# Optimization experiments

Hardware: AMD Instinct MI355X
Metric: run time of the kernel (lower is better)

The kernel has to match this reference:

```python
import jax, jax.numpy as jnp
import numpy as np

B, S, D_MODEL, N_HEADS, D_FF = 4, 2048, 1024, 16, 4096
HEAD_DIM = D_MODEL // N_HEADS
NUM_BUCKETS, MAX_DISTANCE = 32, 128
EPS = 1e-6


def _relative_position_bucket(relative_position, num_buckets=NUM_BUCKETS, max_distance=MAX_DISTANCE):
    # bidirectional (encoder) variant, matching T5RelativePositionBias
    n = -relative_position
    nb = num_buckets // 2
    ret = (n < 0).astype(jnp.int32) * nb
    n = jnp.abs(n)
    max_exact = nb // 2
    val_if_large = max_exact + (
        jnp.log(jnp.maximum(n, 1).astype(jnp.float32) / max_exact)
        / np.log(max_distance / max_exact) * (nb - max_exact)
    ).astype(jnp.int32)
    val_if_large = jnp.minimum(val_if_large, nb - 1)
    return ret + jnp.where(n < max_exact, n, val_if_large)


def t5_position_bias(rel_emb, q_len, k_len):
    ctx = jnp.arange(q_len)[:, None]
    mem = jnp.arange(k_len)[None, :]
    rp_bucket = _relative_position_bucket(mem - ctx)          # [S, S]
    bias = rel_emb[rp_bucket]                                  # [S, S, H]
    return jnp.transpose(bias, (2, 0, 1))[None]                # [1, H, S, S]


def layer_norm(x, g, b):
    mu = jnp.mean(x, axis=-1, keepdims=True)
    var = jnp.mean(jnp.square(x - mu), axis=-1, keepdims=True)
    return (x - mu) * jax.lax.rsqrt(var + EPS) * g + b


def setup_inputs() -> dict:
    key = jax.random.key(0)
    ks = jax.random.split(key, 20)
    s = 0.02
    p = {
        'src': jax.random.normal(ks[0], (B, S, D_MODEL), jnp.float32),
        'wq': jax.random.normal(ks[1], (D_MODEL, D_MODEL), jnp.float32) * s,
        'bq': jnp.zeros((D_MODEL,), jnp.float32),
        'wk': jax.random.normal(ks[2], (D_MODEL, D_MODEL), jnp.float32) * s,
        'bk': jnp.zeros((D_MODEL,), jnp.float32),
        'wv': jax.random.normal(ks[3], (D_MODEL, D_MODEL), jnp.float32) * s,
        'bv': jnp.zeros((D_MODEL,), jnp.float32),
        'wo': jax.random.normal(ks[4], (D_MODEL, D_MODEL), jnp.float32) * s,
        'bo': jnp.zeros((D_MODEL,), jnp.float32),
        'w1': jax.random.normal(ks[5], (D_MODEL, D_FF), jnp.float32) * s,
        'b1': jnp.zeros((D_FF,), jnp.float32),
        'w2': jax.random.normal(ks[6], (D_FF, D_MODEL), jnp.float32) * s,
        'b2': jnp.zeros((D_MODEL,), jnp.float32),
        'ln1_g': jnp.ones((D_MODEL,), jnp.float32),
        'ln1_b': jnp.zeros((D_MODEL,), jnp.float32),
        'ln2_g': jnp.ones((D_MODEL,), jnp.float32),
        'ln2_b': jnp.zeros((D_MODEL,), jnp.float32),
        'rel_emb': jax.random.normal(ks[7], (NUM_BUCKETS, N_HEADS), jnp.float32) * s,
    }
    return p


def reference(src, wq, bq, wk, bk, wv, bv, wo, bo, w1, b1, w2, b2,
              ln1_g, ln1_b, ln2_g, ln2_b, rel_emb):
    b, s, _ = src.shape

    # --- self-attention block (pre-norm) ---
    xn = layer_norm(src, ln1_g, ln1_b)
    q = (xn @ wq + bq).reshape(b, s, N_HEADS, HEAD_DIM).transpose(0, 2, 1, 3)
    k = (xn @ wk + bk).reshape(b, s, N_HEADS, HEAD_DIM).transpose(0, 2, 1, 3)
    v = (xn @ wv + bv).reshape(b, s, N_HEADS, HEAD_DIM).transpose(0, 2, 1, 3)

    bias = t5_position_bias(rel_emb, s, s)                       # [1,H,S,S]
    scores = jnp.einsum('bhqd,bhkd->bhqk', q, k) / np.sqrt(HEAD_DIM) + bias
    attn = jax.nn.softmax(scores, axis=-1)
    ctx = jnp.einsum('bhqk,bhkd->bhqd', attn, v)                 # [B,H,S,Dh]
    ctx = ctx.transpose(0, 2, 1, 3).reshape(b, s, D_MODEL)
    x = src + (ctx @ wo + bo)

    # --- FFN block (pre-norm, ReLU) ---
    yn = layer_norm(x, ln2_g, ln2_b)
    y = jax.nn.relu(yn @ w1 + b1) @ w2 + b2
    return x + y
```

## Files before the change

### kernel.cpp

```cpp
#include <hip/hip_runtime.h>
#include <math.h>

typedef unsigned short u16;

#define S_LEN 2048
#define BSZ 4
#define DM 1024
#define NH 16
#define HD 64
#define DFF 4096
#define ROWS (BSZ * S_LEN)
#define LOG2E 1.4426950408889634f

typedef __attribute__((__ext_vector_type__(8))) __bf16 bf16x8;
typedef __attribute__((__ext_vector_type__(8))) short short8;
typedef __attribute__((__ext_vector_type__(4))) short short4v;
typedef __attribute__((__ext_vector_type__(4))) float f32x4;
typedef __attribute__((__ext_vector_type__(4))) float float4v;

__device__ __forceinline__ float bf2f(u16 u) {
    union { unsigned int i; float f; } c; c.i = ((unsigned int)u) << 16; return c.f;
}
__device__ __forceinline__ u16 f2bf(float f) {
    union { float f; unsigned int i; } c; c.f = f;
    unsigned int r = c.i + 0x7fffu + ((c.i >> 16) & 1u);
    return (u16)(r >> 16);
}
__device__ __forceinline__ u16 f2bf_cvt(float f) {
    __bf16 h = (__bf16)f;
    return __builtin_bit_cast(u16, h);
}
__device__ __forceinline__ float ldin(const void* p, long i, int f32) {
    return f32 ? ((const float*)p)[i] : bf2f(((const u16*)p)[i]);
}
__device__ __forceinline__ int dtype_f32(const u16* ln1g) {
    return ln1g[0] != 0x3F80;
}
__device__ __forceinline__ void gl_lds16(const void* g, void* l) {
    __builtin_amdgcn_global_load_lds(
        (const __attribute__((address_space(1))) unsigned int*)g,
        (__attribute__((address_space(3))) unsigned int*)l, 16, 0, 0);
}

#define BARR  asm volatile("s_barrier" ::: "memory")
#define LGKM0 asm volatile("s_waitcnt lgkmcnt(0)" ::: "memory")
#define VM4   asm volatile("s_waitcnt vmcnt(4)" ::: "memory")
#define VM2   asm volatile("s_waitcnt vmcnt(2)" ::: "memory")
#define VM0   asm volatile("s_waitcnt vmcnt(0)" ::: "memory")

__device__ __forceinline__ void tr_tile(
    const void* __restrict__ src, u16* __restrict__ dst, int N, int K,
    int bx, int by, int f32, int tid, u16 (*t)[72])
{
#pragma unroll
    for (int i = 0; i < 2; i++) {
        int c = tid + i * 256;
        int row = c >> 3, col = (c & 7) * 8;
        long off = (long)(by * 64 + row) * N + bx * 64 + col;
        short8 v;
        if (f32) {
            const float* s = (const float*)src + off;
            float4v a = *(const float4v*)s;
            float4v b = *(const float4v*)(s + 4);
#pragma unroll
            for (int k = 0; k < 4; k++) { v[k] = (short)f2bf(a[k]); v[k + 4] = (short)f2bf(b[k]); }
        } else {
            v = *(const short8*)((const u16*)src + off);
        }
        *(short8*)(&t[row][col]) = v;
    }
    __syncthreads();
#pragma unroll
    for (int i = 0; i < 2; i++) {
        int c = tid + i * 256;
        int row = c >> 3, col = (c & 7) * 8;
        short8 v;
#pragma unroll
        for (int jj = 0; jj < 8; jj++) v[jj] = (short)t[col + jj][row];
        *(short8*)(dst + (long)(bx * 64 + row) * K + by * 64 + col) = v;
    }
}

__global__ __launch_bounds__(256) void prep_all(
    const void* wq, const void* wk, const void* wv, const void* wo,
    const void* w1, const void* w2,
    const void* bq, const void* bk, const void* bv, const void* bo,
    const void* b1, const void* b2, const void* l1g, const void* l1b,
    const void* l2g, const void* l2b, const void* rel,
    const void* src, u16* __restrict__ xn,
    u16* __restrict__ wqkvt, u16* __restrict__ wot,
    u16* __restrict__ w1t, u16* __restrict__ w2t,
    u16* __restrict__ smalls, float* __restrict__ bias_full)
{
    __shared__ u16 t[64][72];
    __shared__ float ps1[4], ps2[4];
    int z = blockIdx.z;
    int f32 = dtype_f32((const u16*)l1g);

    if (z < 4) {
        if (blockIdx.x >= 16) return;
        const void* s = (z == 0) ? wq : (z == 1) ? wk : (z == 2) ? wv : wo;
        u16* dst = (z < 3) ? wqkvt + (long)z * 1024 * 1024 : wot;
        tr_tile(s, dst, DM, DM, blockIdx.x, blockIdx.y, f32, threadIdx.x, t);
        return;
    }
    if (z == 4) {
        tr_tile(w1, w1t, DFF, DM, blockIdx.x, blockIdx.y, f32, threadIdx.x, t);
        return;
    }
    if (z == 5) {
        tr_tile(w2, w2t, DM, DFF, blockIdx.y, blockIdx.x, f32, threadIdx.x, t);
        return;
    }
    if (z == 6) {
        int bidx = blockIdx.y * 64 + blockIdx.x;
        if (bidx >= 256) return;
        int tid = bidx * 256 + threadIdx.x;
        if (tid < 13312) {
            float v;
            if      (tid < 1024)  v = ldin(bq,  tid,         f32);
            else if (tid < 2048)  v = ldin(bk,  tid - 1024,  f32);
            else if (tid < 3072)  v = ldin(bv,  tid - 2048,  f32);
            else if (tid < 4096)  v = ldin(bo,  tid - 3072,  f32);
            else if (tid < 8192)  v = ldin(b1,  tid - 4096,  f32);
            else if (tid < 9216)  v = ldin(b2,  tid - 8192,  f32);
            else if (tid < 10240) v = ldin(l1g, tid - 9216,  f32);
            else if (tid < 11264) v = ldin(l1b, tid - 10240, f32);
            else if (tid < 12288) v = ldin(l2g, tid - 11264, f32);
            else                  v = ldin(l2b, tid - 12288, f32);
            smalls[tid] = f2bf(v);
        }
        if (tid < 4095 * 16) {
            int dIdx = tid >> 4;
            int h = tid & 15;
            int delta = dIdx - 2047;
            int n = -delta;
            int ret = (n < 0) ? 16 : 0;
            int na = (n < 0) ? -n : n;
            int bkt;
            if (na < 8) {
                bkt = na;
            } else {
                float tval = logf((float)na * 0.125f) * 2.8853900817779268f;
                int v = 8 + (int)tval;
                bkt = v < 15 ? v : 15;
            }
            bkt += ret;
            bias_full[h * 4095 + dIdx] = ldin(rel, bkt * 16 + h, f32) * LOG2E;
        }
        return;
    }
    {
        int row = (z - 7) * 1024 + blockIdx.y * 64 + blockIdx.x;
        int tid = threadIdx.x;
        float vals[4];
        if (f32) {
            float4v v = *(const float4v*)((const float*)src + (long)row * DM + tid * 4);
#pragma unroll
            for (int k = 0; k < 4; k++) vals[k] = v[k];
        } else {
            short4v v = *(const short4v*)((const u16*)src + (long)row * DM + tid * 4);
#pragma unroll
            for (int k = 0; k < 4; k++) vals[k] = bf2f((u16)v[k]);
        }
        float s1 = 0.f, s2 = 0.f;
#pragma unroll
        for (int k = 0; k < 4; k++) { s1 += vals[k]; s2 += vals[k] * vals[k]; }
#pragma unroll
        for (int off = 32; off > 0; off >>= 1) {
            s1 += __shfl_xor(s1, off);
            s2 += __shfl_xor(s2, off);
        }
        int wave = tid >> 6, lane = tid & 63;
        if (lane == 0) { ps1[wave] = s1; ps2[wave] = s2; }
        __syncthreads();
        s1 = ps1[0] + ps1[1] + ps1[2] + ps1[3];
        s2 = ps2[0] + ps2[1] + ps2[2] + ps2[3];
        float mu = s1 * (1.0f / DM);
        float var = s2 * (1.0f / DM) - mu * mu;
        float rs = rsqrtf(var + 1e-6f);
        short4v ov;
#pragma unroll
        for (int k = 0; k < 4; k++) {
            float gv = ldin(l1g, tid * 4 + k, f32);
            float bv = ldin(l1b, tid * 4 + k, f32);
            ov[k] = (short)f2bf((vals[k] - mu) * rs * gv + bv);
        }
        *(short4v*)(xn + (long)row * DM + tid * 4) = ov;
    }
}

__global__ __launch_bounds__(256) void ln_kernel(
    const void* __restrict__ xin, int external, const u16* __restrict__ ln1g,
    const u16* __restrict__ g, const u16* __restrict__ bta, u16* __restrict__ out)
{
    int f32 = external ? dtype_f32(ln1g) : 0;
    int row = blockIdx.x;
    int tid = threadIdx.x;
    float vals[4];
    if (f32) {
        float4v v = *(const float4v*)((const float*)xin + (long)row * DM + tid * 4);
#pragma unroll
        for (int k = 0; k < 4; k++) vals[k] = v[k];
    } else {
        short4v v = *(const short4v*)((const u16*)xin + (long)row * DM + tid * 4);
#pragma unroll
        for (int k = 0; k < 4; k++) vals[k] = bf2f((u16)v[k]);
    }
    float s1 = 0.f, s2 = 0.f;
#pragma unroll
    for (int k = 0; k < 4; k++) { s1 += vals[k]; s2 += vals[k] * vals[k]; }
#pragma unroll
    for (int off = 32; off > 0; off >>= 1) {
        s1 += __shfl_xor(s1, off);
        s2 += __shfl_xor(s2, off);
    }
    __shared__ float ps1[4], ps2[4];
    int wave = tid >> 6, lane = tid & 63;
    if (lane == 0) { ps1[wave] = s1; ps2[wave] = s2; }
    __syncthreads();
    s1 = ps1[0] + ps1[1] + ps1[2] + ps1[3];
    s2 = ps2[0] + ps2[1] + ps2[2] + ps2[3];
    float mu = s1 * (1.0f / DM);
    float var = s2 * (1.0f / DM) - mu * mu;
    float rs = rsqrtf(var + 1e-6f);
    short4v ov;
#pragma unroll
    for (int k = 0; k < 4; k++) {
        float gv = bf2f(g[tid * 4 + k]);
        float bv = bf2f(bta[tid * 4 + k]);
        ov[k] = (short)f2bf((vals[k] - mu) * rs * gv + bv);
    }
    *(short4v*)(out + (long)row * DM + tid * 4) = ov;
}

#define TM 256
#define TN 256
#define TK 64

#define PHASE(bi, q, STAGE, WAITV)                                             \
    {                                                                          \
        if ((q) == 0) {                                                        \
            _Pragma("unroll")                                                  \
            for (int j = 0; j < 4; j++) {                                      \
                _Pragma("unroll")                                              \
                for (int t = 0; t < 2; t++)                                    \
                    bfr[j][t] = __builtin_bit_cast(bf16x8, *(const short8*)(   \
                        &Bs[bi][wn * 64 + j * 16 + l16][((t * 4 + quad) ^ rxor) * 8])); \
            }                                                                  \
        }                                                                      \
        _Pragma("unroll")                                                      \
        for (int i = 0; i < 2; i++) {                                          \
            _Pragma("unroll")                                                  \
            for (int t = 0; t < 2; t++)                                        \
                af[i][t] = __builtin_bit_cast(bf16x8, *(const short8*)(        \
                    &As[bi][wm * 128 + ((q) * 2 + i) * 16 + l16][((t * 4 + quad) ^ rxor) * 8])); \
        }                                                                      \
        STAGE                                                                  \
        WAITV;                                                                 \
        BARR;                                                                  \
        LGKM0;                                                                 \
        __builtin_amdgcn_sched_barrier(0);                                     \
        __builtin_amdgcn_s_setprio(1);                                         \
        _Pragma("unroll")                                                      \
        for (int i = 0; i < 2; i++) {                                          \
            _Pragma("unroll")                                                  \
            for (int j = 0; j < 4; j++) {                                      \
                acc[(q) * 2 + i][j] = __builtin_amdgcn_mfma_f32_16x16x32_bf16( \
                    af[i][0], bfr[j][0], acc[(q) * 2 + i][j], 0, 0, 0);        \
                acc[(q) * 2 + i][j] = __builtin_amdgcn_mfma_f32_16x16x32_bf16( \
                    af[i][1], bfr[j][1], acc[(q) * 2 + i][j], 0, 0, 0);        \
            }                                                                  \
        }                                                                      \
        __builtin_amdgcn_s_setprio(0);                                         \
        BARR;                                                                  \
    }

__global__ __launch_bounds__(512, 2) void gemm256(
    const u16* __restrict__ A, const u16* __restrict__ Bt,
    const u16* __restrict__ bias, int M, int N, int K, int mode,
    u16* __restrict__ out_q, u16* __restrict__ out_k, u16* __restrict__ out_v,
    u16* __restrict__ outp)
{
    __shared__ u16 As[2][TM][TK];
    __shared__ u16 Bs[2][TN][TK];

    int tid = threadIdx.x;
    int wavei = tid >> 6, lane = tid & 63;
    int quad = lane >> 4, l16 = lane & 15;
    int wm = wavei >> 2, wn = wavei & 3;

    int nwg = gridDim.x * gridDim.y;
    int bid = blockIdx.y * gridDim.x + blockIdx.x;
    int chunk = nwg >> 3;
    int swz = (bid & 7) * chunk + (bid >> 3);
    int bx = swz % gridDim.x, by = swz / gridDim.x;
    long m0 = (long)by * TM, n0 = (long)bx * TN;

    int srow = tid >> 3;
    int pchk = tid & 7;
    int cchk = pchk ^ (srow & 7);
    int rxor = l16 & 7;

    int NT = K / TK;

    auto stageA = [&](int bufi, int h, int t) {
        const u16* g = A + (m0 + h * 128 + srow) * (long)K + (long)t * TK + cchk * 8;
        gl_lds16(g,                 &As[bufi][h * 128 + srow     ][pchk * 8]);
        gl_lds16(g + 64 * (long)K,  &As[bufi][h * 128 + srow + 64][pchk * 8]);
    };
    auto stageB = [&](int bufi, int h, int t) {
        const u16* g = Bt + (n0 + h * 128 + srow) * (long)K + (long)t * TK + cchk * 8;
        gl_lds16(g,                 &Bs[bufi][h * 128 + srow     ][pchk * 8]);
        gl_lds16(g + 64 * (long)K,  &Bs[bufi][h * 128 + srow + 64][pchk * 8]);
    };

    f32x4 acc[8][4];
    f32x4 z = {0.f, 0.f, 0.f, 0.f};
#pragma unroll
    for (int i = 0; i < 8; i++)
#pragma unroll
        for (int j = 0; j < 4; j++) acc[i][j] = z;

    bf16x8 bfr[4][2];
    bf16x8 af[2][2];

    stageA(0, 0, 0); stageA(0, 1, 0); stageB(0, 0, 0); stageB(0, 1, 0);
    stageB(1, 0, 1); stageB(1, 1, 1);
    VM4;
    BARR;

    for (int kt = 0; kt < NT - 2; kt += 2) {
        PHASE(0, 0, { stageA(1, 0, kt + 1); stageA(1, 1, kt + 1); }, (void)0);
        PHASE(0, 1, { stageB(0, 0, kt + 2); }, (void)0);
        PHASE(0, 2, { stageB(0, 1, kt + 2); }, (void)0);
        PHASE(0, 3, {}, VM4);
        PHASE(1, 0, { stageA(0, 0, kt + 2); }, (void)0);
        PHASE(1, 1, { stageA(0, 1, kt + 2); stageB(1, 0, kt + 3); }, (void)0);
        PHASE(1, 2, { stageB(1, 1, kt + 3); }, (void)0);
        PHASE(1, 3, {}, VM4);
    }
    PHASE(0, 0, { stageA(1, 0, NT - 1); stageA(1, 1, NT - 1); }, (void)0);
    PHASE(0, 1, {}, (void)0);
    PHASE(0, 2, {}, (void)0);
    PHASE(0, 3, {}, VM0);
    PHASE(1, 0, {}, (void)0);
    PHASE(1, 1, {}, (void)0);
    PHASE(1, 2, {}, (void)0);
    PHASE(1, 3, {}, (void)0);

#pragma unroll
    for (int i = 0; i < 8; i++) {
#pragma unroll
        for (int j = 0; j < 4; j++) {
            long gr0 = m0 + wm * 128 + i * 16 + quad * 4;
            long gc = n0 + wn * 64 + j * 16 + l16;
            float bsv = bf2f(bias[gc]);
            if (mode == 1) {
                int sel = (int)(gc >> 10);
                int cc = (int)(gc & 1023);
                int h = cc >> 6, d = cc & 63;
                int b = (int)(gr0 >> 11), s0 = (int)(gr0 & 2047);
                if (sel == 2) {
                    short4v pk;
#pragma unroll
                    for (int r = 0; r < 4; r++)
                        pk[r] = (short)f2bf_cvt(acc[i][j][r] + bsv);
                    *(short4v*)(out_v +
                        (((long)(b * NH + h)) * HD + d) * S_LEN + s0) = pk;
                } else {
                    u16* dst = (sel == 0) ? out_q : out_k;
#pragma unroll
                    for (int r = 0; r < 4; r++)
                        dst[(((long)(b * NH + h)) * S_LEN + s0 + r) * HD + d] =
                            f2bf_cvt(acc[i][j][r] + bsv);
                }
            } else {
#pragma unroll
                for (int r = 0; r < 4; r++) {
                    float val = acc[i][j][r] + bsv;
                    outp[(gr0 + r) * (long)N + gc] = f2bf_cvt(val > 0.f ? val : 0.f);
                }
            }
        }
    }
}

#define NBM 256
#define NBN 128

#define PHN(bi, half, STAGE, WAITV)                                            \
    {                                                                          \
        if ((half) == 0) {                                                     \
            _Pragma("unroll")                                                  \
            for (int j = 0; j < 2; j++) {                                      \
                _Pragma("unroll")                                              \
                for (int t = 0; t < 2; t++)                                    \
                    nbfr[j][t] = __builtin_bit_cast(bf16x8, *(const short8*)(  \
                        &Bs[bi][wn * 32 + j * 16 + l16][((t * 4 + quad) ^ rxor) * 8])); \
            }                                                                  \
        }                                                                      \
        _Pragma("unroll")                                                      \
        for (int i = 0; i < 4; i++) {                                          \
            _Pragma("unroll")                                                  \
            for (int t = 0; t < 2; t++)                                        \
                naf[i][t] = __builtin_bit_cast(bf16x8, *(const short8*)(       \
                    &As[bi][wm * 128 + ((half) * 4 + i) * 16 + l16][((t * 4 + quad) ^ rxor) * 8])); \
        }                                                                      \
        STAGE                                                                  \
        WAITV;                                                                 \
        BARR;                                                                  \
        LGKM0;                                                                 \
        __builtin_amdgcn_sched_barrier(0);                                     \
        __builtin_amdgcn_s_setprio(1);                                         \
        _Pragma("unroll")                                                      \
        for (int i = 0; i < 4; i++) {                                          \
            _Pragma("unroll")                                                  \
            for (int j = 0; j < 2; j++) {                                      \
                acc[(half) * 4 + i][j] = __builtin_amdgcn_mfma_f32_16x16x32_bf16( \
                    naf[i][0], nbfr[j][0], acc[(half) * 4 + i][j], 0, 0, 0);   \
                acc[(half) * 4 + i][j] = __builtin_amdgcn_mfma_f32_16x16x32_bf16( \
                    naf[i][1], nbfr[j][1], acc[(half) * 4 + i][j], 0, 0, 0);   \
            }                                                                  \
        }                                                                      \
        __builtin_amdgcn_s_setprio(0);                                         \
        BARR;                                                                  \
    }

__global__ __launch_bounds__(512, 2) void gemm256n(
    const u16* __restrict__ A, const u16* __restrict__ Bt,
    const u16* __restrict__ bias, int M, int N, int K, int mode,
    const void* __restrict__ res, void* __restrict__ outp,
    const u16* __restrict__ ln1g)
{
    __shared__ u16 As[2][NBM][TK];
    __shared__ u16 Bs[2][NBN][TK];

    int tid = threadIdx.x;
    int wavei = tid >> 6, lane = tid & 63;
    int quad = lane >> 4, l16 = lane & 15;
    int wm = wavei >> 2, wn = wavei & 3;

    int nwg = gridDim.x * gridDim.y;
    int bid = blockIdx.y * gridDim.x + blockIdx.x;
    int chunk = nwg >> 3;
    int swz = (bid & 7) * chunk + (bid >> 3);
    int bx = swz % gridDim.x, by = swz / gridDim.x;
    long m0 = (long)by * NBM, n0 = (long)bx * NBN;
    int flg = dtype_f32(ln1g);

    int srow = tid >> 3;
    int pchk = tid & 7;
    int cchk = pchk ^ (srow & 7);
    int rxor = l16 & 7;

    int NT = K / TK;

    auto stageA = [&](int bufi, int h, int t) {
        const u16* g = A + (m0 + h * 128 + srow) * (long)K + (long)t * TK + cchk * 8;
        gl_lds16(g,                 &As[bufi][h * 128 + srow     ][pchk * 8]);
        gl_lds16(g + 64 * (long)K,  &As[bufi][h * 128 + srow + 64][pchk * 8]);
    };
    auto stageB = [&](int bufi, int t) {
        const u16* g = Bt + (n0 + srow) * (long)K + (long)t * TK + cchk * 8;
        gl_lds16(g,                 &Bs[bufi][srow     ][pchk * 8]);
        gl_lds16(g + 64 * (long)K,  &Bs[bufi][srow + 64][pchk * 8]);
    };

    f32x4 acc[8][2];
    f32x4 z = {0.f, 0.f, 0.f, 0.f};
#pragma unroll
    for (int i = 0; i < 8; i++)
#pragma unroll
        for (int j = 0; j < 2; j++) acc[i][j] = z;

    bf16x8 nbfr[2][2];
    bf16x8 naf[4][2];

    stageA(0, 0, 0); stageA(0, 1, 0); stageB(0, 0);
    stageB(1, 1);
    VM2;
    BARR;

    for (int kt = 0; kt < NT - 2; kt += 2) {
        PHN(0, 0, { stageA(1, 0, kt + 1); stageA(1, 1, kt + 1); }, (void)0);
        PHN(0, 1, { stageB(0, kt + 2); }, VM2);
        PHN(1, 0, { stageA(0, 0, kt + 2); stageA(0, 1, kt + 2); }, (void)0);
        PHN(1, 1, { stageB(1, kt + 3); }, VM2);
    }
    PHN(0, 0, { stageA(1, 0, NT - 1); stageA(1, 1, NT - 1); }, (void)0);
    PHN(0, 1, {}, VM0);
    PHN(1, 0, {}, (void)0);
    PHN(1, 1, {}, (void)0);

#pragma unroll
    for (int i = 0; i < 8; i++) {
#pragma unroll
        for (int j = 0; j < 2; j++) {
#pragma unroll
            for (int r = 0; r < 4; r++) {
                long gr = m0 + wm * 128 + i * 16 + quad * 4 + r;
                long gc = n0 + wn * 32 + j * 16 + l16;
                float val = acc[i][j][r] + bf2f(bias[gc]);
                long idx = gr * (long)N + gc;
                if (mode == 2) {
                    float rv = flg ? ((const float*)res)[idx]
                                   : bf2f(((const u16*)res)[idx]);
                    ((u16*)outp)[idx] = f2bf_cvt(val + rv);
                } else {
                    float o = val + bf2f(((const u16*)res)[idx]);
                    if (flg) ((float*)outp)[idx] = o;
                    else     ((u16*)outp)[idx]  = f2bf_cvt(o);
                }
            }
        }
    }
}

__global__ __launch_bounds__(512, 4) void attn_kernel(
    const u16* __restrict__ Qg, const u16* __restrict__ Kg, const u16* __restrict__ Vtg,
    const float* __restrict__ bias_full, u16* __restrict__ ctx)
{
    __shared__ u16 Ks[64][64];
    __shared__ u16 Vt[64][64];
    __shared__ u16 Ps[128][76];
    __shared__ u16 bias_s[2176];

    int nwg = gridDim.x * gridDim.y;
    int bid = blockIdx.y * gridDim.x + blockIdx.x;
    int chunk = nwg >> 3;
    int swz = (bid & 7) * chunk + (bid >> 3);
    int qt = swz % gridDim.x, bh = swz / gridDim.x;

    int b = bh >> 4, h = bh & 15;
    int q0 = qt * 128;
    const u16* Q  = Qg  + (long)bh * S_LEN * HD;
    const u16* Kp = Kg  + (long)bh * S_LEN * HD;
    const u16* Vp = Vtg + (long)bh * HD * S_LEN;

    int tid = threadIdx.x;
    int wave = tid >> 6, lane = tid & 63;
    int quad = lane >> 4, l16 = lane & 15;

    for (int i = tid; i < 2176; i += 512)
        bias_s[i] = f2bf(bias_full[h * 4095 + 1920 + i - q0]);
    float Bneg = bias_full[h * 4095 + 0];
    float Bpos = bias_full[h * 4095 + 4094];

    int isv = wave >= 4;
    int t2 = tid & 255;
    int prow = t2 >> 3, pchk = t2 & 7;
    int cchk = pchk ^ (prow & 7);
    int rxor = l16 & 7;
    int rc0 = (quad ^ rxor) * 8;
    int rc1 = ((4 + quad) ^ rxor) * 8;

    bf16x8 aq[2];
#pragma unroll
    for (int t = 0; t < 2; t++)
        aq[t] = __builtin_bit_cast(bf16x8,
            *(const short8*)(Q + (long)(q0 + wave * 16 + l16) * HD + t * 32 + quad * 8));

    bf16x8 ones;
#pragma unroll
    for (int i = 0; i < 8; i++) ones[i] = (__bf16)1.0f;

    f32x4 o[4];
    f32x4 z = {0.f, 0.f, 0.f, 0.f};
#pragma unroll
    for (int j = 0; j < 4; j++) o[j] = z;
    f32x4 lacc = z;

    int ib = 127 + quad * 4 - wave * 16 - l16;
    const float c0 = 0.125f * LOG2E;

    auto compute = [&](int t0) {
        f32x4 s_[4];
#pragma unroll
        for (int j = 0; j < 4; j++) {
            f32x4 a = z;
            bf16x8 kf0 = __builtin_bit_cast(bf16x8, *(const short8*)(&Ks[j * 16 + l16][rc0]));
            a = __builtin_amdgcn_mfma_f32_16x16x32_bf16(kf0, aq[0], a, 0, 0, 0);
            bf16x8 kf1 = __builtin_bit_cast(bf16x8, *(const short8*)(&Ks[j * 16 + l16][rc1]));
            a = __builtin_amdgcn_mfma_f32_16x16x32_bf16(kf1, aq[1], a, 0, 0, 0);
            s_[j] = a;
        }
        int d0 = t0 - q0;
        int nearb = (d0 >= -153 && d0 <= 217);
        float bconst = (d0 > 0) ? Bpos : Bneg;
#pragma unroll
        for (int j = 0; j < 4; j++) {
            short4v pk;
#pragma unroll
            for (int r = 0; r < 4; r++) {
                float bl = nearb ? bf2f(bias_s[ib + t0 + j * 16 + r]) : bconst;
                float p = __builtin_amdgcn_exp2f(fmaf(s_[j][r], c0, bl));
                pk[r] = (short)f2bf_cvt(p);
            }
            *(short4v*)(&Ps[wave * 16 + l16][j * 16 + quad * 4]) = pk;
        }
        bf16x8 ap[2];
#pragma unroll
        for (int tt = 0; tt < 2; tt++)
            ap[tt] = __builtin_bit_cast(bf16x8,
                *(const short8*)(&Ps[wave * 16 + l16][tt * 32 + quad * 8]));
        lacc = __builtin_amdgcn_mfma_f32_16x16x32_bf16(ap[0], ones, lacc, 0, 0, 0);
        lacc = __builtin_amdgcn_mfma_f32_16x16x32_bf16(ap[1], ones, lacc, 0, 0, 0);
#pragma unroll
        for (int j = 0; j < 4; j++) {
            f32x4 t = o[j];
            bf16x8 bv0 = __builtin_bit_cast(bf16x8, *(const short8*)(&Vt[j * 16 + l16][rc0]));
            t = __builtin_amdgcn_mfma_f32_16x16x32_bf16(ap[0], bv0, t, 0, 0, 0);
            bf16x8 bv1 = __builtin_bit_cast(bf16x8, *(const short8*)(&Vt[j * 16 + l16][rc1]));
            t = __builtin_amdgcn_mfma_f32_16x16x32_bf16(ap[1], bv1, t, 0, 0, 0);
            o[j] = t;
        }
    };

    auto ld0 = [&](int t) -> short8 {
        return isv ? *(const short8*)(Vp + (long)prow * S_LEN + t + cchk * 8)
                   : *(const short8*)(Kp + (long)(t + prow) * HD + cchk * 8);
    };
    auto ld1 = [&](int t) -> short8 {
        return isv ? *(const short8*)(Vp + (long)(32 + prow) * S_LEN + t + cchk * 8)
                   : *(const short8*)(Kp + (long)(t + 32 + prow) * HD + cchk * 8);
    };
    u16* dst0 = isv ? &Vt[prow][pchk * 8] : &Ks[prow][pchk * 8];
    u16* dst1 = isv ? &Vt[32 + prow][pchk * 8] : &Ks[32 + prow][pchk * 8];

    short8 sa0 = ld0(0), sa1 = ld1(0);
    short8 sb0, sb1;

    for (int t0 = 0; t0 < S_LEN; t0 += 128) {
        if (t0 > 0) BARR;
        VM0;
        *(short8*)dst0 = sa0;
        *(short8*)dst1 = sa1;
        sb0 = ld0(t0 + 64);
        sb1 = ld1(t0 + 64);
        LGKM0; BARR;
        compute(t0);

        BARR;
        VM0;
        *(short8*)dst0 = sb0;
        *(short8*)dst1 = sb1;
        if (t0 + 128 < S_LEN) {
            sa0 = ld0(t0 + 128);
            sa1 = ld1(t0 + 128);
        }
        LGKM0; BARR;
        compute(t0 + 64);
    }

#pragma unroll
    for (int r = 0; r < 4; r++) {
        int qr = wave * 16 + quad * 4 + r;
        float linv = 1.0f / lacc[r];
        long srow2 = (long)(b * S_LEN + q0 + qr);
#pragma unroll
        for (int j = 0; j < 4; j++)
            ctx[srow2 * DM + h * HD + j * 16 + l16] = f2bf_cvt(o[j][r] * linv);
    }
}

extern "C" void kernel_launch(void* const* d_in, const int* in_sizes, int n_in,
                              void* d_out, int out_size, void* d_ws, size_t ws_size,
                              hipStream_t stream)
{
    const void* src  = d_in[0];
    const void* wq   = d_in[1];
    const void* bq   = d_in[2];
    const void* wk   = d_in[3];
    const void* bk   = d_in[4];
    const void* wv   = d_in[5];
    const void* bv   = d_in[6];
    const void* wo   = d_in[7];
    const void* bo   = d_in[8];
    const void* w1   = d_in[9];
    const void* b1   = d_in[10];
    const void* w2   = d_in[11];
    const void* b2   = d_in[12];
    const void* ln1g = d_in[13];
    const void* ln1b = d_in[14];
    const void* ln2g = d_in[15];
    const void* ln2b = d_in[16];
    const void* rel  = d_in[17];
    const u16* l1g16 = (const u16*)ln1g;

    char* ws = (char*)d_ws;
    const long MB = 1L << 20;
    u16*   smalls = (u16*)  (ws);
    float* bfull  = (float*)(ws + 65536);
    u16*   xn     = (u16*)  (ws + 1  * MB);
    u16*   qws    = (u16*)  (ws + 17 * MB);
    u16*   kws    = (u16*)  (ws + 33 * MB);
    u16*   vtg    = (u16*)  (ws + 49 * MB);
    u16*   hbuf   = (u16*)  (ws + 1  * MB);
    u16*   ctx    = (u16*)  (ws + 65 * MB);
    u16*   yn     = (u16*)  (ws + 65 * MB);
    u16*   xbf    = (u16*)  (ws + 81 * MB);
    u16*   wqkvt  = (u16*)  (ws + 97 * MB);
    u16*   wot    = (u16*)  (ws + 103 * MB);
    u16*   w1t    = (u16*)  (ws + 105 * MB);
    u16*   w2t    = (u16*)  (ws + 113 * MB);

    prep_all<<<dim3(64, 16, 15), 256, 0, stream>>>(
        wq, wk, wv, wo, w1, w2, bq, bk, bv, bo, b1, b2,
        ln1g, ln1b, ln2g, ln2b, rel, src, xn,
        wqkvt, wot, w1t, w2t, smalls, bfull);

    gemm256<<<dim3(3072 / TN, ROWS / TM), 512, 0, stream>>>(
        xn, wqkvt, smalls + 0, ROWS, 3072, DM, 1, qws, kws, vtg, nullptr);

    attn_kernel<<<dim3(S_LEN / 128, BSZ * NH), 512, 0, stream>>>(qws, kws, vtg, bfull, ctx);

    gemm256n<<<dim3(DM / NBN, ROWS / NBM), 512, 0, stream>>>(
        ctx, wot, smalls + 3072, ROWS, DM, DM, 2, src, xbf, l1g16);

    ln_kernel<<<ROWS, 256, 0, stream>>>(xbf, 0, l1g16,
                                        smalls + 11264, smalls + 12288, yn);

    gemm256<<<dim3(DFF / TN, ROWS / TM), 512, 0, stream>>>(
        yn, w1t, smalls + 4096, ROWS, DFF, DM, 3, nullptr, nullptr, nullptr, hbuf);

    gemm256n<<<dim3(DM / NBN, ROWS / NBM), 512, 0, stream>>>(
        hbuf, w2t, smalls + 8192, ROWS, DM, DFF, 4, xbf, d_out, l1g16);
}
```

Before: 544.6 us.

## Triple-buffer LDS in gemm256n with three-tile-ahead prefetch

Restructures the main GEMM kernel's K-loop from double-buffered half-phase staging to a triple-buffered pipeline that prefetches tiles three steps ahead. Each iteration consumes one buffer and refills it after its MFMAs, using vmcnt waits tuned to the number of outstanding loads. The goal is to hide more global-to-LDS latency behind compute. The cost is 1.5x the shared memory, which may lower occupancy below the declared 2 blocks per CU, and the irregular rotating buffer index.

```diff
diff --git a/kernel.cpp b/kernel.cpp
--- a/kernel.cpp
+++ b/kernel.cpp
@@ -44,6 +44,9 @@
 
 #define BARR  asm volatile("s_barrier" ::: "memory")
 #define LGKM0 asm volatile("s_waitcnt lgkmcnt(0)" ::: "memory")
+#define VM12  asm volatile("s_waitcnt vmcnt(12)" ::: "memory")
+#define VM8   asm volatile("s_waitcnt vmcnt(8)" ::: "memory")
+#define VM6   asm volatile("s_waitcnt vmcnt(6)" ::: "memory")
 #define VM4   asm volatile("s_waitcnt vmcnt(4)" ::: "memory")
 #define VM2   asm volatile("s_waitcnt vmcnt(2)" ::: "memory")
 #define VM0   asm volatile("s_waitcnt vmcnt(0)" ::: "memory")
@@ -389,52 +392,14 @@
 #define NBM 256
 #define NBN 128
 
-#define PHN(bi, half, STAGE, WAITV)                                            \
-    {                                                                          \
-        if ((half) == 0) {                                                     \
-            _Pragma("unroll")                                                  \
-            for (int j = 0; j < 2; j++) {                                      \
-                _Pragma("unroll")                                              \
-                for (int t = 0; t < 2; t++)                                    \
-                    nbfr[j][t] = __builtin_bit_cast(bf16x8, *(const short8*)(  \
-                        &Bs[bi][wn * 32 + j * 16 + l16][((t * 4 + quad) ^ rxor) * 8])); \
-            }                                                                  \
-        }                                                                      \
-        _Pragma("unroll")                                                      \
-        for (int i = 0; i < 4; i++) {                                          \
-            _Pragma("unroll")                                                  \
-            for (int t = 0; t < 2; t++)                                        \
-                naf[i][t] = __builtin_bit_cast(bf16x8, *(const short8*)(       \
-                    &As[bi][wm * 128 + ((half) * 4 + i) * 16 + l16][((t * 4 + quad) ^ rxor) * 8])); \
-        }                                                                      \
-        STAGE                                                                  \
-        WAITV;                                                                 \
-        BARR;                                                                  \
-        LGKM0;                                                                 \
-        __builtin_amdgcn_sched_barrier(0);                                     \
-        __builtin_amdgcn_s_setprio(1);                                         \
-        _Pragma("unroll")                                                      \
-        for (int i = 0; i < 4; i++) {                                          \
-            _Pragma("unroll")                                                  \
-            for (int j = 0; j < 2; j++) {                                      \
-                acc[(half) * 4 + i][j] = __builtin_amdgcn_mfma_f32_16x16x32_bf16( \
-                    naf[i][0], nbfr[j][0], acc[(half) * 4 + i][j], 0, 0, 0);   \
-                acc[(half) * 4 + i][j] = __builtin_amdgcn_mfma_f32_16x16x32_bf16( \
-                    naf[i][1], nbfr[j][1], acc[(half) * 4 + i][j], 0, 0, 0);   \
-            }                                                                  \
-        }                                                                      \
-        __builtin_amdgcn_s_setprio(0);                                         \
-        BARR;                                                                  \
-    }
-
 __global__ __launch_bounds__(512, 2) void gemm256n(
     const u16* __restrict__ A, const u16* __restrict__ Bt,
     const u16* __restrict__ bias, int M, int N, int K, int mode,
     const void* __restrict__ res, void* __restrict__ outp,
     const u16* __restrict__ ln1g)
 {
-    __shared__ u16 As[2][NBM][TK];
-    __shared__ u16 Bs[2][NBN][TK];
+    __shared__ u16 As[3][NBM][TK];
+    __shared__ u16 Bs[3][NBN][TK];
 
     int tid = threadIdx.x;
     int wavei = tid >> 6, lane = tid & 63;
@@ -456,10 +421,12 @@
 
     int NT = K / TK;
 
-    auto stageA = [&](int bufi, int h, int t) {
-        const u16* g = A + (m0 + h * 128 + srow) * (long)K + (long)t * TK + cchk * 8;
-        gl_lds16(g,                 &As[bufi][h * 128 + srow     ][pchk * 8]);
-        gl_lds16(g + 64 * (long)K,  &As[bufi][h * 128 + srow + 64][pchk * 8]);
+    auto stageA = [&](int bufi, int t) {
+        const u16* g = A + (m0 + srow) * (long)K + (long)t * TK + cchk * 8;
+        gl_lds16(g,                  &As[bufi][srow      ][pchk * 8]);
+        gl_lds16(g +  64 * (long)K,  &As[bufi][srow +  64][pchk * 8]);
+        gl_lds16(g + 128 * (long)K,  &As[bufi][srow + 128][pchk * 8]);
+        gl_lds16(g + 192 * (long)K,  &As[bufi][srow + 192][pchk * 8]);
     };
     auto stageB = [&](int bufi, int t) {
         const u16* g = Bt + (n0 + srow) * (long)K + (long)t * TK + cchk * 8;
@@ -477,21 +444,71 @@
     bf16x8 nbfr[2][2];
     bf16x8 naf[4][2];
 
-    stageA(0, 0, 0); stageA(0, 1, 0); stageB(0, 0);
-    stageB(1, 1);
-    VM2;
+    stageB(0, 0); stageA(0, 0);
+    stageB(1, 1); stageA(1, 1);
+    stageB(2, 2); stageA(2, 2);
+    VM12;
     BARR;
 
-    for (int kt = 0; kt < NT - 2; kt += 2) {
-        PHN(0, 0, { stageA(1, 0, kt + 1); stageA(1, 1, kt + 1); }, (void)0);
-        PHN(0, 1, { stageB(0, kt + 2); }, VM2);
-        PHN(1, 0, { stageA(0, 0, kt + 2); stageA(0, 1, kt + 2); }, (void)0);
-        PHN(1, 1, { stageB(1, kt + 3); }, VM2);
-    }
-    PHN(0, 0, { stageA(1, 0, NT - 1); stageA(1, 1, NT - 1); }, (void)0);
-    PHN(0, 1, {}, VM0);
-    PHN(1, 0, {}, (void)0);
-    PHN(1, 1, {}, (void)0);
+    int ab = 0;
+    for (int t = 0; t < NT; ++t) {
+#pragma unroll
+        for (int j = 0; j < 2; j++)
+#pragma unroll
+            for (int tt = 0; tt < 2; tt++)
+                nbfr[j][tt] = __builtin_bit_cast(bf16x8, *(const short8*)(
+                    &Bs[ab][wn * 32 + j * 16 + l16][((tt * 4 + quad) ^ rxor) * 8]));
+#pragma unroll
+        for (int i = 0; i < 4; i++)
+#pragma unroll
+            for (int tt = 0; tt < 2; tt++)
+                naf[i][tt] = __builtin_bit_cast(bf16x8, *(const short8*)(
+                    &As[ab][wm * 128 + i * 16 + l16][((tt * 4 + quad) ^ rxor) * 8]));
+        LGKM0;
+        BARR;
+        __builtin_amdgcn_sched_barrier(0);
+        __builtin_amdgcn_s_setprio(1);
+#pragma unroll
+        for (int i = 0; i < 4; i++)
+#pragma unroll
+            for (int j = 0; j < 2; j++) {
+                acc[i][j] = __builtin_amdgcn_mfma_f32_16x16x32_bf16(
+                    naf[i][0], nbfr[j][0], acc[i][j], 0, 0, 0);
+                acc[i][j] = __builtin_amdgcn_mfma_f32_16x16x32_bf16(
+                    naf[i][1], nbfr[j][1], acc[i][j], 0, 0, 0);
+            }
+        __builtin_amdgcn_s_setprio(0);
+        if (t + 3 < NT) stageB(ab, t + 3);
+        BARR;
+
+#pragma unroll
+        for (int i = 0; i < 4; i++)
+#pragma unroll
+            for (int tt = 0; tt < 2; tt++)
+                naf[i][tt] = __builtin_bit_cast(bf16x8, *(const short8*)(
+                    &As[ab][wm * 128 + (4 + i) * 16 + l16][((tt * 4 + quad) ^ rxor) * 8]));
+        if (t < NT - 3)      { VM8; }
+        else if (t == NT - 3){ VM6; }
+        else                 { VM0; }
+        LGKM0;
+        BARR;
+        __builtin_amdgcn_sched_barrier(0);
+        __builtin_amdgcn_s_setprio(1);
+#pragma unroll
+        for (int i = 0; i < 4; i++)
+#pragma unroll
+            for (int j = 0; j < 2; j++) {
+                acc[4 + i][j] = __builtin_amdgcn_mfma_f32_16x16x32_bf16(
+                    naf[i][0], nbfr[j][0], acc[4 + i][j], 0, 0, 0);
+                acc[4 + i][j] = __builtin_amdgcn_mfma_f32_16x16x32_bf16(
+                    naf[i][1], nbfr[j][1], acc[4 + i][j], 0, 0, 0);
+            }
+        __builtin_amdgcn_s_setprio(0);
+        if (t + 3 < NT) stageA(ab, t + 3);
+        BARR;
+
+        ab = (ab == 2) ? 0 : ab + 1;
+    }
 
 #pragma unroll
     for (int i = 0; i < 8; i++) {
```

New measurement: 586.6 us. 7.7% more time.
